# Optimization experiments

Hardware: AMD Instinct MI355X
Metric: run time of the kernel (lower is better)

## Reference

```python
import jax, jax.numpy as jnp
import numpy as np
from functools import partial

DX = 0.5
N_STEPS = 8
B, H, W = 8, 512, 512


def _bilinear_interp(vf, pts):
    """Bilinear-batched interpolation of vf (B,2,H,W) at points pts (B,2,H,W).
    pts[:,0] = x coords in [0, W-1], pts[:,1] = y coords in [0, H-1].
    Coordinates are clipped to the image domain (as in torchvf)."""
    Bv, C, Hh, Ww = vf.shape
    x = jnp.clip(pts[:, 0], 0.0, Ww - 1.0)  # (B,H,W)
    y = jnp.clip(pts[:, 1], 0.0, Hh - 1.0)
    x0 = jnp.floor(x)
    y0 = jnp.floor(y)
    wx = (x - x0)[:, None]  # (B,1,H,W) broadcast over channels
    wy = (y - y0)[:, None]
    x0i = x0.astype(jnp.int32)
    y0i = y0.astype(jnp.int32)
    x1i = jnp.minimum(x0i + 1, Ww - 1)
    y1i = jnp.minimum(y0i + 1, Hh - 1)
    vf_flat = vf.reshape(Bv, C, Hh * Ww)

    def gather(yi, xi):
        idx = (yi * Ww + xi).reshape(Bv, 1, Hh * Ww)
        return jnp.take_along_axis(vf_flat, idx, axis=2).reshape(Bv, C, Hh, Ww)

    v00 = gather(y0i, x0i)  # (y0, x0)
    v01 = gather(y0i, x1i)  # (y0, x1)
    v10 = gather(y1i, x0i)  # (y1, x0)
    v11 = gather(y1i, x1i)  # (y1, x1)
    return (v00 * (1.0 - wx) + v01 * wx) * (1.0 - wy) + \
           (v10 * (1.0 - wx) + v11 * wx) * wy


def _init_values(Bv, Hh, Ww, dtype):
    # meshgrid(indexing='ij') -> (y, x); stack(mesh[::-1]) -> (x, y) channel order
    yy, xx = jnp.meshgrid(jnp.arange(Hh), jnp.arange(Ww), indexing='ij')
    init = jnp.stack([xx, yy], axis=0).astype(dtype)  # (2,H,W)
    return jnp.broadcast_to(init[None], (Bv, 2, Hh, Ww))


def _trajectories(vf):
    """Euler integration with stored solutions: (N_STEPS+1, B, 2, H, W)."""
    init = _init_values(*((vf.shape[0],) + vf.shape[2:]), vf.dtype)

    def step(p, _):
        p_next = p + DX * _bilinear_interp(vf, p)
        return p_next, p_next

    _, sols = jax.lax.scan(step, init, None, length=N_STEPS)
    return jnp.concatenate([init[None], sols], axis=0)


def setup_inputs() -> dict:
    key = jax.random.key(0)
    k1, k2 = jax.random.split(key)
    vf_pred = jax.random.normal(k1, (B, 2, H, W), dtype=jnp.float32)
    vf_true = jax.random.normal(k2, (B, 2, H, W), dtype=jnp.float32)
    return {"vf_pred": vf_pred, "vf_true": vf_true}


def reference(vf_pred, vf_true):
    true_traj = _trajectories(vf_true)
    pred_traj = _trajectories(vf_pred)
    # F.mse_loss default reduction='mean'
    return jnp.mean((true_traj - pred_traj) ** 2)
```

## Files before the change

kernel.cpp:

```cpp
#include <hip/hip_runtime.h>
#include <hip/hip_fp16.h>

#define DXC     0.5f
#define NSTEPS  8
#define NPIX    (512 * 512)
#define TOTAL_COUNT 37748736.0

#define TW      64
#define TH      32
#define HX      12
#define HY      8
#define ECOLS   88
#define SST     96
#define EROWS   50
#define TSZ     (EROWS * SST)
#define EMAXU   4700u
#define QPF     (EROWS * 22)
#define QTOT    (2 * QPF)

typedef unsigned int u32;

__device__ __forceinline__ u32 pkrtz(float a, float b) {
    auto h = __builtin_amdgcn_cvt_pkrtz(a, b);
    return __builtin_bit_cast(u32, h);
}

__device__ __forceinline__ float2 h2f2(u32 v) {
    __half2 h = __builtin_bit_cast(__half2, v);
    return make_float2(__low2float(h), __high2float(h));
}

__device__ __forceinline__ void stage_quad(uint2* tT, uint2* tP,
        const float* __restrict__ tbase, const float* __restrict__ pbase,
        int q, int tx0m, int ty0m, bool xin) {
    bool isP = q >= QPF;
    int qq  = isP ? q - QPF : q;
    int row = qq / 22;
    int cq  = (qq - row * 22) * 4;
    int gy  = min(max(ty0m + row, 0), 511);
    const float* c0 = (isP ? pbase : tbase) + (gy << 9);
    const float* c1 = c0 + NPIX;
    float v0[5], v1[5];
    if (xin) {
        int gx = tx0m + cq;
        float4 a = *(const float4*)(c0 + gx);
        float4 b = *(const float4*)(c1 + gx);
        v0[0] = a.x; v0[1] = a.y; v0[2] = a.z; v0[3] = a.w; v0[4] = c0[gx + 4];
        v1[0] = b.x; v1[1] = b.y; v1[2] = b.z; v1[3] = b.w; v1[4] = c1[gx + 4];
    } else {
        #pragma unroll
        for (int j = 0; j < 5; ++j) {
            int gx = min(max(tx0m + cq + j, 0), 511);
            v0[j] = c0[gx]; v1[j] = c1[gx];
        }
    }
    u32 h[5];
    #pragma unroll
    for (int j = 0; j < 5; ++j) h[j] = pkrtz(v0[j], v1[j]);
    uint2* tt  = isP ? tP : tT;
    uint4* dst = (uint4*)(tt + row * SST + cq + (cq >> 4));
    dst[0] = make_uint4(h[0], h[1], h[1], h[2]);
    dst[1] = make_uint4(h[2], h[3], h[3], h[4]);
}

template<bool CLAMP>
__device__ __forceinline__ float2 gather(const uint2* tile,
        float xlo, float xhi, float ylo, float yhi, float fx, float fy) {
    float x = CLAMP ? fminf(fmaxf(fx, xlo), xhi) : fx;
    float y = CLAMP ? fminf(fmaxf(fy, ylo), yhi) : fy;
    float lxf = floorf(x), lyf = floorf(y);
    float wxf = x - lxf,  wyf = y - lyf;
    int lx = (int)lxf, ly = (int)lyf;
    unsigned eu = min((unsigned)(ly * SST + lx + (lx >> 4)), EMAXU);
    uint2 r0 = tile[eu];
    uint2 r1 = tile[eu + SST];
    __half2 wx = __float2half2_rn(wxf);
    __half2 wy = __float2half2_rn(wyf);
    __half2 a0 = __builtin_bit_cast(__half2, r0.x);
    __half2 a1 = __builtin_bit_cast(__half2, r0.y);
    __half2 b0 = __builtin_bit_cast(__half2, r1.x);
    __half2 b1 = __builtin_bit_cast(__half2, r1.y);
    __half2 rt = __hfma2(__hsub2(a1, a0), wx, a0);
    __half2 rb = __hfma2(__hsub2(b1, b0), wx, b0);
    __half2 v  = __hfma2(__hsub2(rb, rt), wy, rt);
    return make_float2(__low2float(v), __high2float(v));
}

template<bool CL>
__device__ __forceinline__ float run_steps(const uint2* tileT, const uint2* tileP,
        float xlo, float xhi, float ylo, float yhi, float px[4], float py[4]) {
    float acc = 0.0f;
    #pragma unroll
    for (int s = 1; s < NSTEPS; ++s) {
        float2 v[4];
        #pragma unroll
        for (int k = 0; k < 4; ++k) {
            const uint2* tl = (k & 1) ? tileP : tileT;
            v[k] = gather<CL>(tl, xlo, xhi, ylo, yhi, px[k], py[k]);
        }
        #pragma unroll
        for (int k = 0; k < 4; ++k) {
            px[k] += DXC * v[k].x;
            py[k] += DXC * v[k].y;
        }
        float dx0 = px[0] - px[1], dy0 = py[0] - py[1];
        float dx1 = px[2] - px[3], dy1 = py[2] - py[3];
        acc += dx0 * dx0 + dy0 * dy0 + dx1 * dx1 + dy1 * dy1;
    }
    return acc;
}

__global__ __launch_bounds__(1024, 8) void ivp_fused_kernel(
        const float* __restrict__ vf_pred,
        const float* __restrict__ vf_true,
        double* __restrict__ ws_part) {
    __shared__ uint2 tileT[TSZ];
    __shared__ uint2 tileP[TSZ];
    __shared__ double sred[16];

    int bid   = blockIdx.x;
    int batch = bid & 7;
    int tile  = bid >> 3;
    int tx0   = (tile & 7) * TW;
    int ty0   = (tile >> 3) * TH;
    int tx0m  = tx0 - HX;
    int ty0m  = ty0 - HY;
    int t = threadIdx.x;

    const float* tbase = vf_true + batch * 2 * NPIX;
    const float* pbase = vf_pred + batch * 2 * NPIX;
    bool xin = (tx0m >= 0) && (tx0m + ECOLS <= 511);

    stage_quad(tileT, tileP, tbase, pbase, t, tx0m, ty0m, xin);
    stage_quad(tileT, tileP, tbase, pbase, t + 1024, tx0m, ty0m, xin);
    if (t < QTOT - 2048)
        stage_quad(tileT, tileP, tbase, pbase, t + 2048, tx0m, ty0m, xin);
    __syncthreads();

    float xlo = (float)(-tx0m), xhi = (float)(511 - tx0m);
    float ylo = (float)(-ty0m), yhi = (float)(511 - ty0m);
    bool interior = (tx0m >= 0) && (tx0m + ECOLS <= 511) &&
                    (ty0m >= 0) && (ty0m + EROWS - 1 <= 511);

    float lx0 = (float)(HX + (t & 63));
    float lyA = (float)(HY + (t >> 6));
    float px[4], py[4];
    px[0] = px[1] = px[2] = px[3] = lx0;
    py[0] = py[1] = lyA;
    py[2] = py[3] = lyA + 16.0f;

    float acc = 0.0f;

    {
        int ilx = HX + (t & 63);
        int e0A = (HY + (t >> 6)) * SST + ilx + (ilx >> 4);
        int e0B = e0A + 16 * SST;
        float2 vT0 = h2f2(tileT[e0A].x);
        float2 vP0 = h2f2(tileP[e0A].x);
        float2 vT1 = h2f2(tileT[e0B].x);
        float2 vP1 = h2f2(tileP[e0B].x);
        px[0] += DXC * vT0.x;  py[0] += DXC * vT0.y;
        px[1] += DXC * vP0.x;  py[1] += DXC * vP0.y;
        px[2] += DXC * vT1.x;  py[2] += DXC * vT1.y;
        px[3] += DXC * vP1.x;  py[3] += DXC * vP1.y;
        float dx0 = px[0] - px[1], dy0 = py[0] - py[1];
        float dx1 = px[2] - px[3], dy1 = py[2] - py[3];
        acc += dx0 * dx0 + dy0 * dy0 + dx1 * dx1 + dy1 * dy1;
    }

    if (interior)
        acc += run_steps<false>(tileT, tileP, xlo, xhi, ylo, yhi, px, py);
    else
        acc += run_steps<true>(tileT, tileP, xlo, xhi, ylo, yhi, px, py);

    double dacc = (double)acc;
    #pragma unroll
    for (int off = 32; off > 0; off >>= 1)
        dacc += __shfl_down(dacc, off, 64);

    int lane = t & 63;
    int wid  = t >> 6;
    if (lane == 0) sred[wid] = dacc;
    __syncthreads();
    if (t == 0) {
        double s = 0.0;
        #pragma unroll
        for (int w = 0; w < 16; ++w) s += sred[w];
        ws_part[bid] = s;
    }
}

__global__ __launch_bounds__(1024) void ivp_finalize_kernel(
        const double* __restrict__ ws_part,
        float* __restrict__ out) {
    __shared__ double sred[16];
    int t = threadIdx.x;
    double d = ws_part[t];
    #pragma unroll
    for (int off = 32; off > 0; off >>= 1)
        d += __shfl_down(d, off, 64);
    if ((t & 63) == 0) sred[t >> 6] = d;
    __syncthreads();
    if (t == 0) {
        double s = 0.0;
        #pragma unroll
        for (int w = 0; w < 16; ++w) s += sred[w];
        out[0] = (float)(s / TOTAL_COUNT);
    }
}

extern "C" void kernel_launch(void* const* d_in, const int* in_sizes, int n_in,
                              void* d_out, int out_size, void* d_ws, size_t ws_size,
                              hipStream_t stream) {
    const float* vf_pred = (const float*)d_in[0];
    const float* vf_true = (const float*)d_in[1];
    float* out = (float*)d_out;
    double* ws_part = (double*)d_ws;

    ivp_fused_kernel<<<1024, 1024, 0, stream>>>(vf_pred, vf_true, ws_part);
    ivp_finalize_kernel<<<1, 1024, 0, stream>>>(ws_part, out);
}
```

Before: 44.07 us.

## Store full 2x2 fp16 bilinear quads per texel and halve tile width

Each shared-memory entry now holds all four corners (two rows by two columns) of the bilinear stencil as one 16-byte uint4, so each gather is a single LDS load instead of two. Tiles shrink to 32x32 pixels with one pixel per thread, so the grid doubles to 2048 blocks and the finalize kernel sums two partials per thread. Padding slots are zeroed to fill the bank-skew gaps. The trade-off is double the shared-memory footprint per pixel, plus more halo redundancy and global re-reads of adjacent rows during staging.

```diff
diff --git a/kernel.cpp b/kernel.cpp
--- a/kernel.cpp
+++ b/kernel.cpp
@@ -6,17 +6,18 @@
 #define NPIX    (512 * 512)
 #define TOTAL_COUNT 37748736.0
 
-#define TW      64
+#define TW      32
 #define TH      32
-#define HX      12
-#define HY      8
-#define ECOLS   88
-#define SST     96
-#define EROWS   50
-#define TSZ     (EROWS * SST)
-#define EMAXU   4700u
-#define QPF     (EROWS * 22)
+#define HX      8
+#define HY      6
+#define ERC     48
+#define ER      44
+#define EPR     54
+#define TSZ     (ER * EPR)
+#define EMAXU   2375u
+#define QPF     (ER * 12)
 #define QTOT    (2 * QPF)
+#define NPAD    (2 * ER * 6)
 
 typedef unsigned int u32;
 
@@ -30,56 +31,68 @@
     return make_float2(__low2float(h), __high2float(h));
 }
 
-__device__ __forceinline__ void stage_quad(uint2* tT, uint2* tP,
-        const float* __restrict__ tbase, const float* __restrict__ pbase,
+__device__ __forceinline__ void stage_quad(uint4* tT, uint4* tP,
+        const float* __restrict__ tb, const float* __restrict__ pb,
         int q, int tx0m, int ty0m, bool xin) {
     bool isP = q >= QPF;
     int qq  = isP ? q - QPF : q;
-    int row = qq / 22;
-    int cq  = (qq - row * 22) * 4;
-    int gy  = min(max(ty0m + row, 0), 511);
-    const float* c0 = (isP ? pbase : tbase) + (gy << 9);
-    const float* c1 = c0 + NPIX;
-    float v0[5], v1[5];
+    int row = qq / 12;
+    int cq  = (qq - row * 12) * 4;
+    int gy0 = min(max(ty0m + row, 0), 511);
+    int gy1 = min(max(ty0m + row + 1, 0), 511);
+    const float* base = isP ? pb : tb;
+    const float* r0c0 = base + (gy0 << 9);
+    const float* r0c1 = r0c0 + NPIX;
+    const float* r1c0 = base + (gy1 << 9);
+    const float* r1c1 = r1c0 + NPIX;
+    float a0[5], a1[5], b0[5], b1[5];
     if (xin) {
         int gx = tx0m + cq;
-        float4 a = *(const float4*)(c0 + gx);
-        float4 b = *(const float4*)(c1 + gx);
-        v0[0] = a.x; v0[1] = a.y; v0[2] = a.z; v0[3] = a.w; v0[4] = c0[gx + 4];
-        v1[0] = b.x; v1[1] = b.y; v1[2] = b.z; v1[3] = b.w; v1[4] = c1[gx + 4];
+        float4 va = *(const float4*)(r0c0 + gx);
+        float4 vb = *(const float4*)(r0c1 + gx);
+        float4 vc = *(const float4*)(r1c0 + gx);
+        float4 vd = *(const float4*)(r1c1 + gx);
+        a0[0]=va.x; a0[1]=va.y; a0[2]=va.z; a0[3]=va.w; a0[4]=r0c0[gx+4];
+        a1[0]=vb.x; a1[1]=vb.y; a1[2]=vb.z; a1[3]=vb.w; a1[4]=r0c1[gx+4];
+        b0[0]=vc.x; b0[1]=vc.y; b0[2]=vc.z; b0[3]=vc.w; b0[4]=r1c0[gx+4];
+        b1[0]=vd.x; b1[1]=vd.y; b1[2]=vd.z; b1[3]=vd.w; b1[4]=r1c1[gx+4];
     } else {
         #pragma unroll
         for (int j = 0; j < 5; ++j) {
             int gx = min(max(tx0m + cq + j, 0), 511);
-            v0[j] = c0[gx]; v1[j] = c1[gx];
+            a0[j] = r0c0[gx]; a1[j] = r0c1[gx];
+            b0[j] = r1c0[gx]; b1[j] = r1c1[gx];
         }
     }
-    u32 h[5];
-    #pragma unroll
-    for (int j = 0; j < 5; ++j) h[j] = pkrtz(v0[j], v1[j]);
-    uint2* tt  = isP ? tP : tT;
-    uint4* dst = (uint4*)(tt + row * SST + cq + (cq >> 4));
-    dst[0] = make_uint4(h[0], h[1], h[1], h[2]);
-    dst[1] = make_uint4(h[2], h[3], h[3], h[4]);
+    u32 ht[5], hb[5];
+    #pragma unroll
+    for (int j = 0; j < 5; ++j) {
+        ht[j] = pkrtz(a0[j], a1[j]);
+        hb[j] = pkrtz(b0[j], b1[j]);
+    }
+    uint4* dst = (isP ? tP : tT) + row * EPR + cq + (cq >> 3);
+    dst[0] = make_uint4(ht[0], ht[1], hb[0], hb[1]);
+    dst[1] = make_uint4(ht[1], ht[2], hb[1], hb[2]);
+    dst[2] = make_uint4(ht[2], ht[3], hb[2], hb[3]);
+    dst[3] = make_uint4(ht[3], ht[4], hb[3], hb[4]);
 }
 
 template<bool CLAMP>
-__device__ __forceinline__ float2 gather(const uint2* tile,
+__device__ __forceinline__ float2 gatherQ(const uint4* tile,
         float xlo, float xhi, float ylo, float yhi, float fx, float fy) {
     float x = CLAMP ? fminf(fmaxf(fx, xlo), xhi) : fx;
     float y = CLAMP ? fminf(fmaxf(fy, ylo), yhi) : fy;
     float lxf = floorf(x), lyf = floorf(y);
     float wxf = x - lxf,  wyf = y - lyf;
     int lx = (int)lxf, ly = (int)lyf;
-    unsigned eu = min((unsigned)(ly * SST + lx + (lx >> 4)), EMAXU);
-    uint2 r0 = tile[eu];
-    uint2 r1 = tile[eu + SST];
+    unsigned eu = min((unsigned)(ly * EPR + lx + (lx >> 3)), EMAXU);
+    uint4 q = tile[eu];
     __half2 wx = __float2half2_rn(wxf);
     __half2 wy = __float2half2_rn(wyf);
-    __half2 a0 = __builtin_bit_cast(__half2, r0.x);
-    __half2 a1 = __builtin_bit_cast(__half2, r0.y);
-    __half2 b0 = __builtin_bit_cast(__half2, r1.x);
-    __half2 b1 = __builtin_bit_cast(__half2, r1.y);
+    __half2 a0 = __builtin_bit_cast(__half2, q.x);
+    __half2 a1 = __builtin_bit_cast(__half2, q.y);
+    __half2 b0 = __builtin_bit_cast(__half2, q.z);
+    __half2 b1 = __builtin_bit_cast(__half2, q.w);
     __half2 rt = __hfma2(__hsub2(a1, a0), wx, a0);
     __half2 rb = __hfma2(__hsub2(b1, b0), wx, b0);
     __half2 v  = __hfma2(__hsub2(rb, rt), wy, rt);
@@ -87,25 +100,18 @@
 }
 
 template<bool CL>
-__device__ __forceinline__ float run_steps(const uint2* tileT, const uint2* tileP,
-        float xlo, float xhi, float ylo, float yhi, float px[4], float py[4]) {
+__device__ __forceinline__ float run_steps(const uint4* tileT, const uint4* tileP,
+        float xlo, float xhi, float ylo, float yhi,
+        float& xT, float& yT, float& xP, float& yP) {
     float acc = 0.0f;
     #pragma unroll
     for (int s = 1; s < NSTEPS; ++s) {
-        float2 v[4];
-        #pragma unroll
-        for (int k = 0; k < 4; ++k) {
-            const uint2* tl = (k & 1) ? tileP : tileT;
-            v[k] = gather<CL>(tl, xlo, xhi, ylo, yhi, px[k], py[k]);
-        }
-        #pragma unroll
-        for (int k = 0; k < 4; ++k) {
-            px[k] += DXC * v[k].x;
-            py[k] += DXC * v[k].y;
-        }
-        float dx0 = px[0] - px[1], dy0 = py[0] - py[1];
-        float dx1 = px[2] - px[3], dy1 = py[2] - py[3];
-        acc += dx0 * dx0 + dy0 * dy0 + dx1 * dx1 + dy1 * dy1;
+        float2 vT = gatherQ<CL>(tileT, xlo, xhi, ylo, yhi, xT, yT);
+        float2 vP = gatherQ<CL>(tileP, xlo, xhi, ylo, yhi, xP, yP);
+        xT += DXC * vT.x;  yT += DXC * vT.y;
+        xP += DXC * vP.x;  yP += DXC * vP.y;
+        float dx = xT - xP, dy = yT - yP;
+        acc += dx * dx + dy * dy;
     }
     return acc;
 }
@@ -114,64 +120,60 @@
         const float* __restrict__ vf_pred,
         const float* __restrict__ vf_true,
         double* __restrict__ ws_part) {
-    __shared__ uint2 tileT[TSZ];
-    __shared__ uint2 tileP[TSZ];
+    __shared__ uint4 tileT[TSZ];
+    __shared__ uint4 tileP[TSZ];
     __shared__ double sred[16];
 
     int bid   = blockIdx.x;
     int batch = bid & 7;
     int tile  = bid >> 3;
-    int tx0   = (tile & 7) * TW;
-    int ty0   = (tile >> 3) * TH;
+    int tx0   = (tile & 15) * TW;
+    int ty0   = (tile >> 4) * TH;
     int tx0m  = tx0 - HX;
     int ty0m  = ty0 - HY;
     int t = threadIdx.x;
 
-    const float* tbase = vf_true + batch * 2 * NPIX;
-    const float* pbase = vf_pred + batch * 2 * NPIX;
-    bool xin = (tx0m >= 0) && (tx0m + ECOLS <= 511);
-
-    stage_quad(tileT, tileP, tbase, pbase, t, tx0m, ty0m, xin);
-    stage_quad(tileT, tileP, tbase, pbase, t + 1024, tx0m, ty0m, xin);
-    if (t < QTOT - 2048)
-        stage_quad(tileT, tileP, tbase, pbase, t + 2048, tx0m, ty0m, xin);
+    const float* tb = vf_true + batch * 2 * NPIX;
+    const float* pb = vf_pred + batch * 2 * NPIX;
+    bool xin = (tx0m >= 0) && (tx0m + ERC <= 511);
+
+    if (t < NPAD) {
+        bool isP = t >= NPAD / 2;
+        int  pt  = isP ? t - NPAD / 2 : t;
+        int  r   = pt / 6;
+        int  k   = pt - r * 6;
+        (isP ? tileP : tileT)[r * EPR + 9 * k + 8] = make_uint4(0, 0, 0, 0);
+    }
+    stage_quad(tileT, tileP, tb, pb, t, tx0m, ty0m, xin);
+    if (t < QTOT - 1024)
+        stage_quad(tileT, tileP, tb, pb, t + 1024, tx0m, ty0m, xin);
     __syncthreads();
 
     float xlo = (float)(-tx0m), xhi = (float)(511 - tx0m);
     float ylo = (float)(-ty0m), yhi = (float)(511 - ty0m);
-    bool interior = (tx0m >= 0) && (tx0m + ECOLS <= 511) &&
-                    (ty0m >= 0) && (ty0m + EROWS - 1 <= 511);
-
-    float lx0 = (float)(HX + (t & 63));
-    float lyA = (float)(HY + (t >> 6));
-    float px[4], py[4];
-    px[0] = px[1] = px[2] = px[3] = lx0;
-    py[0] = py[1] = lyA;
-    py[2] = py[3] = lyA + 16.0f;
+    bool interior = xin && (ty0m >= 0) && (ty0m + ER <= 511);
+
+    int ilx = HX + (t & 31);
+    int ily = HY + (t >> 5);
+    float xT = (float)ilx, yT = (float)ily;
+    float xP = xT, yP = yT;
 
     float acc = 0.0f;
 
     {
-        int ilx = HX + (t & 63);
-        int e0A = (HY + (t >> 6)) * SST + ilx + (ilx >> 4);
-        int e0B = e0A + 16 * SST;
-        float2 vT0 = h2f2(tileT[e0A].x);
-        float2 vP0 = h2f2(tileP[e0A].x);
-        float2 vT1 = h2f2(tileT[e0B].x);
-        float2 vP1 = h2f2(tileP[e0B].x);
-        px[0] += DXC * vT0.x;  py[0] += DXC * vT0.y;
-        px[1] += DXC * vP0.x;  py[1] += DXC * vP0.y;
-        px[2] += DXC * vT1.x;  py[2] += DXC * vT1.y;
-        px[3] += DXC * vP1.x;  py[3] += DXC * vP1.y;
-        float dx0 = px[0] - px[1], dy0 = py[0] - py[1];
-        float dx1 = px[2] - px[3], dy1 = py[2] - py[3];
-        acc += dx0 * dx0 + dy0 * dy0 + dx1 * dx1 + dy1 * dy1;
+        int e0 = ily * EPR + ilx + (ilx >> 3);
+        float2 vT = h2f2(tileT[e0].x);
+        float2 vP = h2f2(tileP[e0].x);
+        xT += DXC * vT.x;  yT += DXC * vT.y;
+        xP += DXC * vP.x;  yP += DXC * vP.y;
+        float dx = xT - xP, dy = yT - yP;
+        acc += dx * dx + dy * dy;
     }
 
     if (interior)
-        acc += run_steps<false>(tileT, tileP, xlo, xhi, ylo, yhi, px, py);
+        acc += run_steps<false>(tileT, tileP, xlo, xhi, ylo, yhi, xT, yT, xP, yP);
     else
-        acc += run_steps<true>(tileT, tileP, xlo, xhi, ylo, yhi, px, py);
+        acc += run_steps<true>(tileT, tileP, xlo, xhi, ylo, yhi, xT, yT, xP, yP);
 
     double dacc = (double)acc;
     #pragma unroll
@@ -195,7 +197,7 @@
         float* __restrict__ out) {
     __shared__ double sred[16];
     int t = threadIdx.x;
-    double d = ws_part[t];
+    double d = ws_part[t] + ws_part[t + 1024];
     #pragma unroll
     for (int off = 32; off > 0; off >>= 1)
         d += __shfl_down(d, off, 64);
@@ -217,6 +219,6 @@
     float* out = (float*)d_out;
     double* ws_part = (double*)d_ws;
 
-    ivp_fused_kernel<<<1024, 1024, 0, stream>>>(vf_pred, vf_true, ws_part);
+    ivp_fused_kernel<<<2048, 1024, 0, stream>>>(vf_pred, vf_true, ws_part);
     ivp_finalize_kernel<<<1, 1024, 0, stream>>>(ws_part, out);
 }
```

New measurement: 49.32 us. +11.9%, slower.
